# Kernel tuning notes

Hardware: AMD Instinct MI355X
Metric: run time of the kernel (lower is better)

Reference implementation:

```python
import jax, jax.numpy as jnp
import numpy as np

# Model config (matches init_kwargs)
HIDDEN = 2048
N_HEADS = 32
N_KV_HEADS = 8
HEAD_DIM = 64
BS = 8  # block_size_x = block_size_y = block_size_z


def setup_inputs() -> dict:
    key = jax.random.key(0)
    ks = jax.random.split(key, 5)
    B, X, Y, Z = 2, 16, 16, 16
    L = X * Y * Z  # 4096
    s = 1.0 / np.sqrt(HIDDEN)
    return {
        "hidden_states": jax.random.normal(ks[0], (B, L, HIDDEN), jnp.float32),
        "Wq": jax.random.normal(ks[1], (N_HEADS * HEAD_DIM, HIDDEN), jnp.float32) * s,
        "Wk": jax.random.normal(ks[2], (N_KV_HEADS * HEAD_DIM, HIDDEN), jnp.float32) * s,
        "Wv": jax.random.normal(ks[3], (N_KV_HEADS * HEAD_DIM, HIDDEN), jnp.float32) * s,
        "Wo": jax.random.normal(ks[4], (HIDDEN, N_HEADS * HEAD_DIM), jnp.float32) * s,
        "x_dim": 16,
        "y_dim": 16,
        "z_dim": 16,
    }


def _to_blocks(t, B, x_dim, y_dim, z_dim, H):
    # t: [B, L, H*D] with L interpreted as (x, y, z) row-major grid.
    # einops: 'b (bnx bsx bny bsy bnz bsz) (h d) -> (b bnx bny bnz) (bsx bsy bsz) h d'
    bnx, bny, bnz = x_dim // BS, y_dim // BS, z_dim // BS
    t = t.reshape(B, bnx, BS, bny, BS, bnz, BS, H, HEAD_DIM)
    t = t.transpose(0, 1, 3, 5, 2, 4, 6, 7, 8)  # [B,bnx,bny,bnz,bsx,bsy,bsz,H,D]
    return t.reshape(B * bnx * bny * bnz, BS * BS * BS, H, HEAD_DIM)


def _from_blocks(o, B, x_dim, y_dim, z_dim):
    bnx, bny, bnz = x_dim // BS, y_dim // BS, z_dim // BS
    o = o.reshape(B, bnx, bny, bnz, BS, BS, BS, N_HEADS, HEAD_DIM)
    o = o.transpose(0, 1, 4, 2, 5, 3, 6, 7, 8)  # back to (bnx bsx bny bsy bnz bsz)
    return o.reshape(B, x_dim * y_dim * z_dim, N_HEADS * HEAD_DIM)


def reference(hidden_states, Wq, Wk, Wv, Wo, x_dim, y_dim, z_dim):
    B, L, _ = hidden_states.shape
    q = _to_blocks(hidden_states @ Wq.T, B, x_dim, y_dim, z_dim, N_HEADS)     # [NB,T,H,D]
    k = _to_blocks(hidden_states @ Wk.T, B, x_dim, y_dim, z_dim, N_KV_HEADS)  # [NB,T,Hk,D]
    v = _to_blocks(hidden_states @ Wv.T, B, x_dim, y_dim, z_dim, N_KV_HEADS)
    # GQA: repeat kv heads across groups (flash_attn handles this internally)
    g = N_HEADS // N_KV_HEADS
    k = jnp.repeat(k, g, axis=2)
    v = jnp.repeat(v, g, axis=2)
    scale = HEAD_DIM ** -0.5
    # non-causal full attention within each 3D block
    scores = jnp.einsum('bthd,bshd->bhts', q, k) * scale  # [NB,H,T,T]
    p = jax.nn.softmax(scores, axis=-1)
    o = jnp.einsum('bhts,bshd->bthd', p, v)               # [NB,T,H,D]
    o = _from_blocks(o, B, x_dim, y_dim, z_dim)           # [B,L,H*D]
    return o @ Wo.T
```

## Files before the change

### kernel.cpp

```cpp
#include <hip/hip_runtime.h>

typedef _Float16 f16;
typedef _Float16 f16x4 __attribute__((ext_vector_type(4)));
typedef _Float16 f16x8 __attribute__((ext_vector_type(8)));
typedef float f32x4 __attribute__((ext_vector_type(4)));
typedef unsigned int u32;
typedef u32 u32x4 __attribute__((ext_vector_type(4)));

__device__ __forceinline__ f32x4 mfma16(f16x8 a, f16x8 b, f32x4 c) {
  return __builtin_amdgcn_mfma_f32_16x16x32_f16(a, b, c, 0, 0, 0);
}

__device__ __forceinline__ void gld_lds16(const void* g, void* l) {
  __builtin_amdgcn_global_load_lds(
      (const __attribute__((address_space(1))) void*)g,
      (__attribute__((address_space(3))) void*)l, 16, 0, 0);
}

__device__ __forceinline__ u32 pkrtz(float a, float b) {
  return __builtin_bit_cast(u32, __builtin_amdgcn_cvt_pkrtz(a, b));
}

#define XSWZ(row) (((row) & 7) << 4)

__global__ __launch_bounds__(256) void cast5_k(
    const float4* s0, const float4* s1, const float4* s2, const float4* s3,
    const float4* s4, f16x4* d0, f16x4* d1, f16x4* d2, f16x4* d3, f16x4* d4,
    int e0, int e1, int e2, int e3, int e4) {
  int i = blockIdx.x * blockDim.x + threadIdx.x;
  int stride = gridDim.x * blockDim.x;
  for (; i < e4; i += stride) {
    const float4* s = s0; f16x4* d = d0; int base = 0;
    if (i >= e0) { s = s1; d = d1; base = e0; }
    if (i >= e1) { s = s2; d = d2; base = e1; }
    if (i >= e2) { s = s3; d = d3; base = e2; }
    if (i >= e3) { s = s4; d = d4; base = e3; }
    float4 v = s[i - base];
    f16x4 o;
    o.x = (f16)v.x; o.y = (f16)v.y; o.z = (f16)v.z; o.w = (f16)v.w;
    d[i - base] = o;
  }
}

template <typename OutT>
__global__ __launch_bounds__(256, 2) void gemm_bt(
    const f16* __restrict__ A, const f16* __restrict__ B, OutT* __restrict__ C,
    int M, int N, int K, float oscale) {
  __shared__ __align__(16) f16 Al[128 * 64];
  __shared__ __align__(16) f16 Bl[128 * 64];
  const int tid = threadIdx.x;
  const int lane = tid & 63;
  const int wave = tid >> 6;
  const int bm = blockIdx.x, bn = blockIdx.y;
  const int wm = wave >> 1, wn = wave & 1;
  f32x4 acc[4][4] = {};

  const size_t ldb = (size_t)K * 2;
  const char* Ab = (const char*)A + (size_t)bm * 128 * ldb;
  const char* Bb = (const char*)B + (size_t)bn * 128 * ldb;

  const int kTiles = K >> 6;
  for (int kt = 0; kt < kTiles; ++kt) {
    const size_t kOff = (size_t)kt << 7;
    __syncthreads();
#pragma unroll
    for (int i = 0; i < 4; ++i) {
      int c = i * 256 + tid;
      int row = c >> 3;
      int colb = ((c & 7) << 4) ^ XSWZ(row);
      gld_lds16(Ab + (size_t)row * ldb + kOff + colb,
                (char*)Al + (i * 256 + wave * 64) * 16);
      gld_lds16(Bb + (size_t)row * ldb + kOff + colb,
                (char*)Bl + (i * 256 + wave * 64) * 16);
    }
    __syncthreads();
#pragma unroll
    for (int kk = 0; kk < 2; ++kk) {
      const int kb = kk * 64 + ((lane >> 4) << 4);
      f16x8 af[4], bf[4];
#pragma unroll
      for (int mf = 0; mf < 4; ++mf) {
        int row = wm * 64 + mf * 16 + (lane & 15);
        af[mf] = *(const f16x8*)((const char*)Al + (row << 7) + (kb ^ XSWZ(row)));
      }
#pragma unroll
      for (int nf = 0; nf < 4; ++nf) {
        int row = wn * 64 + nf * 16 + (lane & 15);
        bf[nf] = *(const f16x8*)((const char*)Bl + (row << 7) + (kb ^ XSWZ(row)));
      }
#pragma unroll
      for (int mf = 0; mf < 4; ++mf)
#pragma unroll
        for (int nf = 0; nf < 4; ++nf)
          acc[mf][nf] = mfma16(af[mf], bf[nf], acc[mf][nf]);
    }
  }
  const int r0 = ((lane >> 4) << 2);
  const int cl = lane & 15;
#pragma unroll
  for (int mf = 0; mf < 4; ++mf)
#pragma unroll
    for (int r = 0; r < 4; ++r) {
      size_t row = (size_t)bm * 128 + wm * 64 + mf * 16 + r0 + r;
#pragma unroll
      for (int nf = 0; nf < 4; ++nf) {
        int col = bn * 128 + wn * 64 + nf * 16 + cl;
        C[row * N + col] = (OutT)(acc[mf][nf][r] * oscale);
      }
    }
}

template <typename OutT>
__global__ __launch_bounds__(512, 2) void gemm_bt8(
    const f16* __restrict__ A, const f16* __restrict__ B, OutT* __restrict__ C,
    int M, int N, int K, float oscale) {
  __shared__ __align__(16) char lds[131072];
  const int tid = threadIdx.x;
  const int lane = tid & 63;
  const int wave = tid >> 6;
  const int wm = wave >> 2, wn = wave & 3;
  const int l15 = lane & 15, g = lane >> 4;
  const int bid = blockIdx.x;
  const int bm = (bid & 7) * 4 + ((bid >> 3) & 3);
  const int bn = bid >> 5;

  const size_t ldb = (size_t)K * 2;
  const int r0 = tid >> 2, r1 = 128 + (tid >> 2);
  const int chx = (((tid & 3) ^ ((tid >> 3) & 3)) << 4);
  const char* As0 = (const char*)A + (size_t)(bm * 256 + r0) * ldb + chx;
  const char* As1 = (const char*)A + (size_t)(bm * 256 + r1) * ldb + chx;
  const char* Bs0 = (const char*)B + (size_t)(bn * 256 + r0) * ldb + chx;
  const char* Bs1 = (const char*)B + (size_t)(bn * 256 + r1) * ldb + chx;

  auto stA = [&](int buf, int t, int kh) {
    char* dst = (char*)lds + (buf * 2 + kh) * 16384 + wave * 1024;
    size_t ko = (size_t)t * 128 + (size_t)kh * 64;
    gld_lds16(As0 + ko, dst);
    gld_lds16(As1 + ko, dst + 8192);
  };
  auto stB = [&](int buf, int t, int kh) {
    char* dst = (char*)lds + 65536 + (buf * 2 + kh) * 16384 + wave * 1024;
    size_t ko = (size_t)t * 128 + (size_t)kh * 64;
    gld_lds16(Bs0 + ko, dst);
    gld_lds16(Bs1 + ko, dst + 8192);
  };

  int aoff[8], boff[4];
  const int rsw = (g ^ ((l15 >> 1) & 3)) << 4;
#pragma unroll
  for (int mf = 0; mf < 8; ++mf)
    aoff[mf] = (wm * 128 + mf * 16 + l15) * 64 + rsw;
#pragma unroll
  for (int nf = 0; nf < 4; ++nf)
    boff[nf] = (wn * 64 + nf * 16 + l15) * 64 + rsw;

  f32x4 acc[8][4] = {};

  stA(0, 0, 0); stB(0, 0, 0); stA(0, 0, 1); stB(0, 0, 1);
  stA(1, 1, 0); stB(1, 1, 0); stA(1, 1, 1);
  asm volatile("s_waitcnt vmcnt(6)" ::: "memory");
  __builtin_amdgcn_s_barrier();

  const int nkt = K >> 6;
  for (int T = 0; T < nkt; ++T) {
    const int cur = T & 1;
    const char* A0 = (const char*)lds + (cur * 2 + 0) * 16384;
    const char* A1 = (const char*)lds + (cur * 2 + 1) * 16384;
    const char* B0r = (const char*)lds + 65536 + (cur * 2 + 0) * 16384;
    const char* B1r = (const char*)lds + 65536 + (cur * 2 + 1) * 16384;
    f16x8 a[8], b0, b1;
#pragma unroll
    for (int mf = 0; mf < 8; ++mf) a[mf] = *(const f16x8*)(A0 + aoff[mf]);
    b0 = *(const f16x8*)(B0r + boff[0]);
    b1 = *(const f16x8*)(B0r + boff[1]);
    if (T + 1 < nkt) stB(cur ^ 1, T + 1, 1);
    __builtin_amdgcn_s_barrier();
    __builtin_amdgcn_s_setprio(1);
#pragma unroll
    for (int mf = 0; mf < 8; ++mf) {
      acc[mf][0] = mfma16(a[mf], b0, acc[mf][0]);
      acc[mf][1] = mfma16(a[mf], b1, acc[mf][1]);
    }
    __builtin_amdgcn_s_setprio(0);
    __builtin_amdgcn_s_barrier();
    b0 = *(const f16x8*)(B0r + boff[2]);
    b1 = *(const f16x8*)(B0r + boff[3]);
    if (T + 2 < nkt) stA(cur, T + 2, 0);
    __builtin_amdgcn_s_barrier();
    __builtin_amdgcn_s_setprio(1);
#pragma unroll
    for (int mf = 0; mf < 8; ++mf) {
      acc[mf][2] = mfma16(a[mf], b0, acc[mf][2]);
      acc[mf][3] = mfma16(a[mf], b1, acc[mf][3]);
    }
    __builtin_amdgcn_s_setprio(0);
    __builtin_amdgcn_s_barrier();
#pragma unroll
    for (int mf = 0; mf < 8; ++mf) a[mf] = *(const f16x8*)(A1 + aoff[mf]);
    b0 = *(const f16x8*)(B1r + boff[0]);
    b1 = *(const f16x8*)(B1r + boff[1]);
    if (T + 2 < nkt) stB(cur, T + 2, 0);
    __builtin_amdgcn_s_barrier();
    __builtin_amdgcn_s_setprio(1);
#pragma unroll
    for (int mf = 0; mf < 8; ++mf) {
      acc[mf][0] = mfma16(a[mf], b0, acc[mf][0]);
      acc[mf][1] = mfma16(a[mf], b1, acc[mf][1]);
    }
    __builtin_amdgcn_s_setprio(0);
    __builtin_amdgcn_s_barrier();
    b0 = *(const f16x8*)(B1r + boff[2]);
    b1 = *(const f16x8*)(B1r + boff[3]);
    if (T + 2 < nkt) stA(cur, T + 2, 1);
    if (T < nkt - 2) asm volatile("s_waitcnt vmcnt(6)" ::: "memory");
    else             asm volatile("s_waitcnt vmcnt(0)" ::: "memory");
    __builtin_amdgcn_s_barrier();
    __builtin_amdgcn_s_setprio(1);
#pragma unroll
    for (int mf = 0; mf < 8; ++mf) {
      acc[mf][2] = mfma16(a[mf], b0, acc[mf][2]);
      acc[mf][3] = mfma16(a[mf], b1, acc[mf][3]);
    }
    __builtin_amdgcn_s_setprio(0);
    __builtin_amdgcn_s_barrier();
  }
#pragma unroll
  for (int mf = 0; mf < 8; ++mf)
#pragma unroll
    for (int r = 0; r < 4; ++r) {
      size_t row = (size_t)bm * 256 + wm * 128 + mf * 16 + g * 4 + r;
#pragma unroll
      for (int nf = 0; nf < 4; ++nf) {
        int col = bn * 256 + wn * 64 + nf * 16 + l15;
        C[row * (size_t)N + col] = (OutT)(acc[mf][nf][r] * oscale);
      }
    }
}

__device__ __forceinline__ int tok_row(int nb, int t) {
  int b = nb >> 3;
  int x = (((nb >> 2) & 1) << 3) | (t >> 6);
  int y = (((nb >> 1) & 1) << 3) | ((t >> 3) & 7);
  int z = ((nb & 1) << 3) | (t & 7);
  return (b << 12) | (x << 8) | (y << 4) | z;
}

__global__ __launch_bounds__(256) void attn3d(
    const f16* __restrict__ Q, const f16* __restrict__ KV, f16* __restrict__ O) {
  __shared__ __align__(16) f16 Ql[128 * 64];
  __shared__ __align__(16) f16 Kl[64 * 64];
  __shared__ __align__(16) f16 Vt[64 * 64];
  const int tid = threadIdx.x;
  const int lane = tid & 63;
  const int wave = tid >> 6;
  const int fid = blockIdx.x;
  const int orig = (fid & 7) * 256 + (fid >> 3);
  const int qt = orig & 3, h = (orig >> 2) & 31, nb = orig >> 7;
  const int hk = h >> 2;
  const int l15 = lane & 15;
  const int g = lane >> 4;
  const size_t ldkv = 2048;

  const int pos2 = (((lane & 3) | (((lane >> 4) & 1) << 2) |
                     (((lane >> 2) & 3) << 3) | ((lane >> 5) << 5))) * 2;

#pragma unroll
  for (int i = 0; i < 4; ++i) {
    int c = i * 256 + tid;
    int row = c >> 3;
    int colb = ((c & 7) << 4) ^ XSWZ(row);
    gld_lds16((const char*)Q + (size_t)tok_row(nb, qt * 128 + row) * 4096 + h * 128 + colb,
              (char*)Ql + (i * 256 + wave * 64) * 16);
  }
  __syncthreads();
  f16x8 bq[2][2];
#pragma unroll
  for (int qf = 0; qf < 2; ++qf)
#pragma unroll
    for (int kk = 0; kk < 2; ++kk) {
      int row = wave * 32 + qf * 16 + l15;
      int kb = kk * 64 + (g << 4);
      bq[qf][kk] = *(const f16x8*)((const char*)Ql + (row << 7) + (kb ^ XSWZ(row)));
    }

  f32x4 o[2][4] = {};
  float lacc[2] = {0.f, 0.f};

  for (int kt = 0; kt < 8; ++kt) {
    f16x8 vch[2];
#pragma unroll
    for (int it = 0; it < 2; ++it) {
      int idx = it * 256 + tid;
      int kv = idx & 63, dc = idx >> 6;
      vch[it] = *(const f16x8*)((const char*)KV +
          (size_t)tok_row(nb, kt * 64 + kv) * ldkv + 1024 + hk * 128 + dc * 16);
    }
    __syncthreads();
#pragma unroll
    for (int i = 0; i < 2; ++i) {
      int c = i * 256 + tid;
      int row = c >> 3;
      int colb = ((c & 7) << 4) ^ XSWZ(row);
      gld_lds16((const char*)KV + (size_t)tok_row(nb, kt * 64 + row) * ldkv + hk * 128 + colb,
                (char*)Kl + (i * 256 + wave * 64) * 16);
    }
#pragma unroll
    for (int it = 0; it < 2; ++it) {
      const int dbase = (it * 4 + wave) * 8;
#pragma unroll
      for (int j = 0; j < 8; ++j)
        *(f16*)((char*)Vt + ((dbase + j) << 7) + (pos2 ^ (j << 4))) = vch[it][j];
    }
    __syncthreads();
    f32x4 s[2][4] = {};
    __builtin_amdgcn_s_setprio(1);
#pragma unroll
    for (int kk = 0; kk < 2; ++kk) {
      const int kb = kk * 64 + (g << 4);
      f16x8 ka[4];
#pragma unroll
      for (int nf = 0; nf < 4; ++nf) {
        int krow = nf * 16 + l15;
        ka[nf] = *(const f16x8*)((const char*)Kl + (krow << 7) + (kb ^ XSWZ(krow)));
      }
#pragma unroll
      for (int qf = 0; qf < 2; ++qf)
#pragma unroll
        for (int nf = 0; nf < 4; ++nf)
          s[qf][nf] = mfma16(ka[nf], bq[qf][kk], s[qf][nf]);
    }
    __builtin_amdgcn_s_setprio(0);
#pragma unroll
    for (int qf = 0; qf < 2; ++qf) {
      float ls = 0.f;
#pragma unroll
      for (int nf = 0; nf < 4; ++nf)
#pragma unroll
        for (int r = 0; r < 4; ++r) {
          float p = __builtin_amdgcn_exp2f(s[qf][nf][r]);
          s[qf][nf][r] = p;
          ls += p;
        }
      lacc[qf] += ls;
    }
    __builtin_amdgcn_s_setprio(1);
#pragma unroll
    for (int kh = 0; kh < 2; ++kh) {
      f16x8 va[4];
      const int cb = kh * 64 + g * 16;
#pragma unroll
      for (int df = 0; df < 4; ++df) {
        int d = df * 16 + l15;
        va[df] = *(const f16x8*)((const char*)Vt + (d << 7) + (cb ^ XSWZ(d)));
      }
#pragma unroll
      for (int qf = 0; qf < 2; ++qf) {
        u32x4 pw = {pkrtz(s[qf][2 * kh][0], s[qf][2 * kh][1]),
                    pkrtz(s[qf][2 * kh][2], s[qf][2 * kh][3]),
                    pkrtz(s[qf][2 * kh + 1][0], s[qf][2 * kh + 1][1]),
                    pkrtz(s[qf][2 * kh + 1][2], s[qf][2 * kh + 1][3])};
        f16x8 pf = __builtin_bit_cast(f16x8, pw);
#pragma unroll
        for (int df = 0; df < 4; ++df)
          o[qf][df] = mfma16(va[df], pf, o[qf][df]);
      }
    }
    __builtin_amdgcn_s_setprio(0);
  }
#pragma unroll
  for (int qf = 0; qf < 2; ++qf) {
    float l = lacc[qf];
    l += __shfl_xor(l, 16);
    l += __shfl_xor(l, 32);
    float inv = 1.f / l;
    int t = qt * 128 + wave * 32 + qf * 16 + l15;
    char* dst = (char*)O + (size_t)tok_row(nb, t) * 4096 + h * 128;
#pragma unroll
    for (int df = 0; df < 4; ++df) {
      f16x4 o4;
#pragma unroll
      for (int r = 0; r < 4; ++r) o4[r] = (f16)(o[qf][df][r] * inv);
      *(f16x4*)(dst + df * 32 + g * 8) = o4;
    }
  }
}

extern "C" void kernel_launch(void* const* d_in, const int* in_sizes, int n_in,
                              void* d_out, int out_size, void* d_ws, size_t ws_size,
                              hipStream_t stream) {
  (void)in_sizes; (void)n_in; (void)out_size; (void)ws_size;
  const float* hs = (const float*)d_in[0];
  const float* Wq = (const float*)d_in[1];
  const float* Wk = (const float*)d_in[2];
  const float* Wv = (const float*)d_in[3];
  const float* Wo = (const float*)d_in[4];
  float* out = (float*)d_out;
  char* ws = (char*)d_ws;

  f16* hid16 = (f16*)(ws + 0);
  f16* Wq16  = (f16*)(ws + 33554432);
  f16* Wk16  = (f16*)(ws + 41943040);
  f16* Wv16  = (f16*)(ws + 44040192);
  f16* Wo16  = (f16*)(ws + 46137344);
  f16* Q16   = (f16*)(ws + 54525952);
  f16* KV16  = (f16*)(ws + 88080384);

  cast5_k<<<2048, 256, 0, stream>>>(
      (const float4*)hs, (const float4*)Wq, (const float4*)Wk,
      (const float4*)Wv, (const float4*)Wo,
      (f16x4*)hid16, (f16x4*)Wq16, (f16x4*)Wk16, (f16x4*)Wv16, (f16x4*)Wo16,
      4194304, 5242880, 5505024, 5767168, 6815744);

  gemm_bt8<f16><<<256, 512, 0, stream>>>(hid16, Wq16, Q16, 8192, 2048, 2048,
                                         0.18033688011112042f);
  gemm_bt<f16><<<dim3(64, 8), 256, 0, stream>>>(hid16, Wk16, KV16, 8192, 1024, 2048, 1.0f);

  attn3d<<<2048, 256, 0, stream>>>(Q16, KV16, hid16);

  gemm_bt8<float><<<256, 512, 0, stream>>>(hid16, Wo16, out, 8192, 2048, 2048, 1.0f);
}
```

Before: 273.2 us.

## Double-buffer MFMA fragments in registers across LDS phases of GEMM loop

Reorganizes the GEMM main loop so A and B fragments are ping-ponged between two register sets (aE/aO, bX/bY). The next phase's LDS reads are issued before the barrier while the current 4x4 MFMA cluster runs, instead of loading and then computing serially. The loop is unrolled by two so LDS buffer indices are compile-time constants. This raises VGPR pressure and assumes an even K-tile count; the final iteration also issues one harmless extra read of stale LDS.

```diff
diff --git a/kernel.cpp b/kernel.cpp
--- a/kernel.cpp
+++ b/kernel.cpp
@@ -155,75 +155,76 @@
     boff[nf] = (wn * 64 + nf * 16 + l15) * 64 + rsw;
 
   f32x4 acc[8][4] = {};
+  f16x8 aE[4], aO[4], bX[4], bY[4];
 
   stA(0, 0, 0); stB(0, 0, 0); stA(0, 0, 1); stB(0, 0, 1);
   stA(1, 1, 0); stB(1, 1, 0); stA(1, 1, 1);
   asm volatile("s_waitcnt vmcnt(6)" ::: "memory");
   __builtin_amdgcn_s_barrier();
+#pragma unroll
+  for (int j = 0; j < 4; ++j) aE[j] = *(const f16x8*)(lds + aoff[j]);
+#pragma unroll
+  for (int j = 0; j < 4; ++j) bX[j] = *(const f16x8*)(lds + 65536 + boff[j]);
 
   const int nkt = K >> 6;
-  for (int T = 0; T < nkt; ++T) {
-    const int cur = T & 1;
-    const char* A0 = (const char*)lds + (cur * 2 + 0) * 16384;
-    const char* A1 = (const char*)lds + (cur * 2 + 1) * 16384;
-    const char* B0r = (const char*)lds + 65536 + (cur * 2 + 0) * 16384;
-    const char* B1r = (const char*)lds + 65536 + (cur * 2 + 1) * 16384;
-    f16x8 a[8], b0, b1;
-#pragma unroll
-    for (int mf = 0; mf < 8; ++mf) a[mf] = *(const f16x8*)(A0 + aoff[mf]);
-    b0 = *(const f16x8*)(B0r + boff[0]);
-    b1 = *(const f16x8*)(B0r + boff[1]);
-    if (T + 1 < nkt) stB(cur ^ 1, T + 1, 1);
-    __builtin_amdgcn_s_barrier();
-    __builtin_amdgcn_s_setprio(1);
-#pragma unroll
-    for (int mf = 0; mf < 8; ++mf) {
-      acc[mf][0] = mfma16(a[mf], b0, acc[mf][0]);
-      acc[mf][1] = mfma16(a[mf], b1, acc[mf][1]);
-    }
-    __builtin_amdgcn_s_setprio(0);
-    __builtin_amdgcn_s_barrier();
-    b0 = *(const f16x8*)(B0r + boff[2]);
-    b1 = *(const f16x8*)(B0r + boff[3]);
-    if (T + 2 < nkt) stA(cur, T + 2, 0);
-    __builtin_amdgcn_s_barrier();
-    __builtin_amdgcn_s_setprio(1);
-#pragma unroll
-    for (int mf = 0; mf < 8; ++mf) {
-      acc[mf][2] = mfma16(a[mf], b0, acc[mf][2]);
-      acc[mf][3] = mfma16(a[mf], b1, acc[mf][3]);
-    }
-    __builtin_amdgcn_s_setprio(0);
-    __builtin_amdgcn_s_barrier();
-#pragma unroll
-    for (int mf = 0; mf < 8; ++mf) a[mf] = *(const f16x8*)(A1 + aoff[mf]);
-    b0 = *(const f16x8*)(B1r + boff[0]);
-    b1 = *(const f16x8*)(B1r + boff[1]);
-    if (T + 2 < nkt) stB(cur, T + 2, 0);
-    __builtin_amdgcn_s_barrier();
-    __builtin_amdgcn_s_setprio(1);
-#pragma unroll
-    for (int mf = 0; mf < 8; ++mf) {
-      acc[mf][0] = mfma16(a[mf], b0, acc[mf][0]);
-      acc[mf][1] = mfma16(a[mf], b1, acc[mf][1]);
-    }
-    __builtin_amdgcn_s_setprio(0);
-    __builtin_amdgcn_s_barrier();
-    b0 = *(const f16x8*)(B1r + boff[2]);
-    b1 = *(const f16x8*)(B1r + boff[3]);
-    if (T + 2 < nkt) stA(cur, T + 2, 1);
-    if (T < nkt - 2) asm volatile("s_waitcnt vmcnt(6)" ::: "memory");
-    else             asm volatile("s_waitcnt vmcnt(0)" ::: "memory");
-    __builtin_amdgcn_s_barrier();
-    __builtin_amdgcn_s_setprio(1);
-#pragma unroll
-    for (int mf = 0; mf < 8; ++mf) {
-      acc[mf][2] = mfma16(a[mf], b0, acc[mf][2]);
-      acc[mf][3] = mfma16(a[mf], b1, acc[mf][3]);
-    }
-    __builtin_amdgcn_s_setprio(0);
-    __builtin_amdgcn_s_barrier();
-  }
+
+#define MFMA_CLUST(aset, bset, m0)                               \
+  __builtin_amdgcn_s_setprio(1);                                 \
+  _Pragma("unroll") for (int mf = 0; mf < 4; ++mf)               \
+  _Pragma("unroll") for (int nf = 0; nf < 4; ++nf)               \
+    acc[m0 + mf][nf] = mfma16(aset[mf], bset[nf], acc[m0 + mf][nf]); \
+  __builtin_amdgcn_s_setprio(0);
+
+#define TILE(CUR)                                                           \
+  do {                                                                      \
+    const char* A0c = lds + ((CUR)*2 + 0) * 16384;                          \
+    const char* A1c = lds + ((CUR)*2 + 1) * 16384;                          \
+    const char* B1c = lds + 65536 + ((CUR)*2 + 1) * 16384;                  \
+    const char* A0n = lds + (((CUR) ^ 1) * 2 + 0) * 16384;                  \
+    const char* B0n = lds + 65536 + (((CUR) ^ 1) * 2 + 0) * 16384;          \
+                   \
+    if (T + 1 < nkt) stB((CUR) ^ 1, T + 1, 1);                              \
+    _Pragma("unroll") for (int j = 0; j < 4; ++j)                           \
+        aO[j] = *(const f16x8*)(A0c + aoff[4 + j]);                         \
+    __builtin_amdgcn_s_barrier();                                           \
+    MFMA_CLUST(aE, bX, 0)                                                   \
+    __builtin_amdgcn_s_barrier();                                           \
+           \
+    if (T + 2 < nkt) stA((CUR), T + 2, 0);                                  \
+    _Pragma("unroll") for (int j = 0; j < 4; ++j)                           \
+        aE[j] = *(const f16x8*)(A1c + aoff[j]);                             \
+    _Pragma("unroll") for (int j = 0; j < 4; ++j)                           \
+        bY[j] = *(const f16x8*)(B1c + boff[j]);                             \
+    __builtin_amdgcn_s_barrier();                                           \
+    MFMA_CLUST(aO, bX, 4)                                                   \
+    __builtin_amdgcn_s_barrier();                                           \
+                   \
+    if (T + 2 < nkt) stB((CUR), T + 2, 0);                                  \
+    _Pragma("unroll") for (int j = 0; j < 4; ++j)                           \
+        aO[j] = *(const f16x8*)(A1c + aoff[4 + j]);                         \
+    __builtin_amdgcn_s_barrier();                                           \
+    MFMA_CLUST(aE, bY, 0)                                                   \
+    __builtin_amdgcn_s_barrier();                                           \
+       \
+    if (T + 2 < nkt) stA((CUR), T + 2, 1);                                  \
+    if (T < nkt - 2) asm volatile("s_waitcnt vmcnt(6)" ::: "memory");       \
+    else             asm volatile("s_waitcnt vmcnt(0)" ::: "memory");       \
+    _Pragma("unroll") for (int j = 0; j < 4; ++j)                           \
+        aE[j] = *(const f16x8*)(A0n + aoff[j]);                             \
+    _Pragma("unroll") for (int j = 0; j < 4; ++j)                           \
+        bX[j] = *(const f16x8*)(B0n + boff[j]);                             \
+    __builtin_amdgcn_s_barrier();                                           \
+    MFMA_CLUST(aO, bY, 4)                                                   \
+    __builtin_amdgcn_s_barrier();                                           \
+  } while (0)
+
+  for (int T2 = 0; T2 < nkt; T2 += 2) {
+    { int T = T2;     TILE(0); }
+    { int T = T2 + 1; TILE(1); }
+  }
+#undef TILE
+#undef MFMA_CLUST
+
 #pragma unroll
   for (int mf = 0; mf < 8; ++mf)
 #pragma unroll
```

Result: slower. 348.2 us (+27.4%).

## Process all 512 queries per block-head in one attention workgroup

Applied to the files above, without the earlier changes.

Each attention workgroup now handles a full 512-query block for one head using 8 waves with 64 queries per wave, where before four workgroups each handled 128 queries. K/V tiles are loaded into LDS once per (block, head) instead of four times, which cuts global traffic and LDS staging. The cost is higher register use (doubled accumulators and packed P), a larger Q LDS buffer (64KB), and only 512 workgroups, which may lower occupancy.

```diff
diff --git a/kernel.cpp b/kernel.cpp
--- a/kernel.cpp
+++ b/kernel.cpp
@@ -245,17 +245,17 @@
   return (b << 12) | (x << 8) | (y << 4) | z;
 }
 
-__global__ __launch_bounds__(256) void attn3d(
+__global__ __launch_bounds__(512) void attn3d(
     const f16* __restrict__ Q, const f16* __restrict__ KV, f16* __restrict__ O) {
-  __shared__ __align__(16) f16 Ql[128 * 64];
+  __shared__ __align__(16) f16 Ql[512 * 64];
   __shared__ __align__(16) f16 Kl[64 * 64];
   __shared__ __align__(16) f16 Vt[64 * 64];
   const int tid = threadIdx.x;
   const int lane = tid & 63;
   const int wave = tid >> 6;
   const int fid = blockIdx.x;
-  const int orig = (fid & 7) * 256 + (fid >> 3);
-  const int qt = orig & 3, h = (orig >> 2) & 31, nb = orig >> 7;
+  const int orig = (fid & 7) * 64 + (fid >> 3);
+  const int h = orig & 31, nb = orig >> 5;
   const int hk = h >> 2;
   const int l15 = lane & 15;
   const int g = lane >> 4;
@@ -265,54 +265,46 @@
                      (((lane >> 2) & 3) << 3) | ((lane >> 5) << 5))) * 2;
 
 #pragma unroll
-  for (int i = 0; i < 4; ++i) {
-    int c = i * 256 + tid;
+  for (int i = 0; i < 8; ++i) {
+    int c = i * 512 + tid;
     int row = c >> 3;
     int colb = ((c & 7) << 4) ^ XSWZ(row);
-    gld_lds16((const char*)Q + (size_t)tok_row(nb, qt * 128 + row) * 4096 + h * 128 + colb,
-              (char*)Ql + (i * 256 + wave * 64) * 16);
+    gld_lds16((const char*)Q + (size_t)tok_row(nb, row) * 4096 + h * 128 + colb,
+              (char*)Ql + (i * 512 + wave * 64) * 16);
   }
   __syncthreads();
-  f16x8 bq[2][2];
-#pragma unroll
-  for (int qf = 0; qf < 2; ++qf)
+  f16x8 bq[4][2];
+#pragma unroll
+  for (int qf = 0; qf < 4; ++qf)
 #pragma unroll
     for (int kk = 0; kk < 2; ++kk) {
-      int row = wave * 32 + qf * 16 + l15;
+      int row = wave * 64 + qf * 16 + l15;
       int kb = kk * 64 + (g << 4);
       bq[qf][kk] = *(const f16x8*)((const char*)Ql + (row << 7) + (kb ^ XSWZ(row)));
     }
 
-  f32x4 o[2][4] = {};
-  float lacc[2] = {0.f, 0.f};
+  f32x4 o[4][4] = {};
+  float lacc[4] = {0.f, 0.f, 0.f, 0.f};
 
   for (int kt = 0; kt < 8; ++kt) {
-    f16x8 vch[2];
-#pragma unroll
-    for (int it = 0; it < 2; ++it) {
-      int idx = it * 256 + tid;
-      int kv = idx & 63, dc = idx >> 6;
-      vch[it] = *(const f16x8*)((const char*)KV +
-          (size_t)tok_row(nb, kt * 64 + kv) * ldkv + 1024 + hk * 128 + dc * 16);
-    }
+    const int kv = tid & 63, dc = tid >> 6;
+    f16x8 vch = *(const f16x8*)((const char*)KV +
+        (size_t)tok_row(nb, kt * 64 + kv) * ldkv + 1024 + hk * 128 + dc * 16);
     __syncthreads();
-#pragma unroll
-    for (int i = 0; i < 2; ++i) {
-      int c = i * 256 + tid;
-      int row = c >> 3;
-      int colb = ((c & 7) << 4) ^ XSWZ(row);
+    {
+      int row = tid >> 3;
+      int colb = ((tid & 7) << 4) ^ XSWZ(row);
       gld_lds16((const char*)KV + (size_t)tok_row(nb, kt * 64 + row) * ldkv + hk * 128 + colb,
-                (char*)Kl + (i * 256 + wave * 64) * 16);
-    }
-#pragma unroll
-    for (int it = 0; it < 2; ++it) {
-      const int dbase = (it * 4 + wave) * 8;
+                (char*)Kl + (wave * 64) * 16);
+    }
+    {
+      const int dbase = wave * 8;
 #pragma unroll
       for (int j = 0; j < 8; ++j)
-        *(f16*)((char*)Vt + ((dbase + j) << 7) + (pos2 ^ (j << 4))) = vch[it][j];
+        *(f16*)((char*)Vt + ((dbase + j) << 7) + (pos2 ^ (j << 4))) = vch[j];
     }
     __syncthreads();
-    f32x4 s[2][4] = {};
+    f32x4 s[4][4] = {};
     __builtin_amdgcn_s_setprio(1);
 #pragma unroll
     for (int kk = 0; kk < 2; ++kk) {
@@ -324,14 +316,15 @@
         ka[nf] = *(const f16x8*)((const char*)Kl + (krow << 7) + (kb ^ XSWZ(krow)));
       }
 #pragma unroll
-      for (int qf = 0; qf < 2; ++qf)
+      for (int qf = 0; qf < 4; ++qf)
 #pragma unroll
         for (int nf = 0; nf < 4; ++nf)
           s[qf][nf] = mfma16(ka[nf], bq[qf][kk], s[qf][nf]);
     }
     __builtin_amdgcn_s_setprio(0);
-#pragma unroll
-    for (int qf = 0; qf < 2; ++qf) {
+    u32x4 pf[4][2];
+#pragma unroll
+    for (int qf = 0; qf < 4; ++qf) {
       float ls = 0.f;
 #pragma unroll
       for (int nf = 0; nf < 4; ++nf)
@@ -342,6 +335,12 @@
           ls += p;
         }
       lacc[qf] += ls;
+#pragma unroll
+      for (int kh = 0; kh < 2; ++kh)
+        pf[qf][kh] = u32x4{pkrtz(s[qf][2 * kh][0], s[qf][2 * kh][1]),
+                           pkrtz(s[qf][2 * kh][2], s[qf][2 * kh][3]),
+                           pkrtz(s[qf][2 * kh + 1][0], s[qf][2 * kh + 1][1]),
+                           pkrtz(s[qf][2 * kh + 1][2], s[qf][2 * kh + 1][3])};
     }
     __builtin_amdgcn_s_setprio(1);
 #pragma unroll
@@ -354,26 +353,22 @@
         va[df] = *(const f16x8*)((const char*)Vt + (d << 7) + (cb ^ XSWZ(d)));
       }
 #pragma unroll
-      for (int qf = 0; qf < 2; ++qf) {
-        u32x4 pw = {pkrtz(s[qf][2 * kh][0], s[qf][2 * kh][1]),
-                    pkrtz(s[qf][2 * kh][2], s[qf][2 * kh][3]),
-                    pkrtz(s[qf][2 * kh + 1][0], s[qf][2 * kh + 1][1]),
-                    pkrtz(s[qf][2 * kh + 1][2], s[qf][2 * kh + 1][3])};
-        f16x8 pf = __builtin_bit_cast(f16x8, pw);
+      for (int qf = 0; qf < 4; ++qf) {
+        f16x8 pfh = __builtin_bit_cast(f16x8, pf[qf][kh]);
 #pragma unroll
         for (int df = 0; df < 4; ++df)
-          o[qf][df] = mfma16(va[df], pf, o[qf][df]);
-      }
-    }
-    __builtin_amdgcn_s_setprio(0);
-  }
-#pragma unroll
-  for (int qf = 0; qf < 2; ++qf) {
+          o[qf][df] = mfma16(va[df], pfh, o[qf][df]);
+      }
+    }
+    __builtin_amdgcn_s_setprio(0);
+  }
+#pragma unroll
+  for (int qf = 0; qf < 4; ++qf) {
     float l = lacc[qf];
     l += __shfl_xor(l, 16);
     l += __shfl_xor(l, 32);
     float inv = 1.f / l;
-    int t = qt * 128 + wave * 32 + qf * 16 + l15;
+    int t = wave * 64 + qf * 16 + l15;
     char* dst = (char*)O + (size_t)tok_row(nb, t) * 4096 + h * 128;
 #pragma unroll
     for (int df = 0; df < 4; ++df) {
@@ -415,7 +410,7 @@
                                          0.18033688011112042f);
   gemm_bt<f16><<<dim3(64, 8), 256, 0, stream>>>(hid16, Wk16, KV16, 8192, 1024, 2048, 1.0f);
 
-  attn3d<<<2048, 256, 0, stream>>>(Q16, KV16, hid16);
+  attn3d<<<512, 512, 0, stream>>>(Q16, KV16, hid16);
 
   gemm_bt8<float><<<256, 512, 0, stream>>>(hid16, Wo16, out, 8192, 2048, 2048, 1.0f);
 }
```

New measurement: 269.4 us. No clear change (-1.4%).
